# Kernel tuning notes

Measured on AMD Instinct MI355X. Metric: run time of the kernel, lower is better.

The kernel has to match this reference:

```python
import jax, jax.numpy as jnp
import numpy as np

DIM = 768
NUM_HEADS = 16
D_K = DIM // NUM_HEADS


def setup_inputs() -> dict:
    key = jax.random.key(0)
    ks = jax.random.split(key, 9)
    B, T = 4, 2048
    s = 1.0 / np.sqrt(DIM)
    return {
        "x": jax.random.normal(ks[0], (B, T, DIM), dtype=jnp.float32),
        "Wq": jax.random.normal(ks[1], (DIM, DIM), dtype=jnp.float32) * s,
        "bq": jnp.zeros((DIM,), dtype=jnp.float32),
        "Wk": jax.random.normal(ks[2], (DIM, DIM), dtype=jnp.float32) * s,
        "bk": jnp.zeros((DIM,), dtype=jnp.float32),
        "Wv": jax.random.normal(ks[3], (DIM, DIM), dtype=jnp.float32) * s,
        "bv": jnp.zeros((DIM,), dtype=jnp.float32),
        "Wp": jax.random.normal(ks[4], (DIM, DIM), dtype=jnp.float32) * s,
        "bp": jnp.zeros((DIM,), dtype=jnp.float32),
    }


def reference(x, Wq, bq, Wk, bk, Wv, bv, Wp, bp):
    B, T, _ = x.shape
    # QKV projections (weights stored as [in, out])
    q = x @ Wq + bq
    k = x @ Wk + bk
    v = x @ Wv + bv
    # split heads: (B, H, T, d_k)
    q = q.reshape(B, T, NUM_HEADS, D_K).transpose(0, 2, 1, 3)
    k = k.reshape(B, T, NUM_HEADS, D_K).transpose(0, 2, 1, 3)
    v = v.reshape(B, T, NUM_HEADS, D_K).transpose(0, 2, 1, 3)
    # scaled dot-product attention; dropout omitted (eval mode)
    scores = jnp.einsum("bhtd,bhsd->bhts", q, k) / jnp.sqrt(jnp.float32(D_K))
    attn = jax.nn.softmax(scores, axis=-1)
    out = jnp.einsum("bhts,bhsd->bhtd", attn, v)
    out = out.transpose(0, 2, 1, 3).reshape(B, T, DIM)
    return out @ Wp + bp
```

## Files before the change

### kernel.cpp

```cpp
#include <hip/hip_runtime.h>
#include <math.h>

#define T_SEQ 2048
#define B_SZ  4
#define DIM   768
#define NH    16
#define DK    48
#define NQK   1536
#define N3    2304
#define LDP   72

typedef __bf16 bf16x8 __attribute__((ext_vector_type(8)));
typedef float  f32x4  __attribute__((ext_vector_type(4)));

__device__ __forceinline__ unsigned short f32_to_bf16(float f) {
    unsigned u = __float_as_uint(f);
    u += 0x7FFFu + ((u >> 16) & 1u);
    return (unsigned short)(u >> 16);
}
__device__ __forceinline__ unsigned pack_bf16x2(float a, float b) {
    return (unsigned)f32_to_bf16(a) | ((unsigned)f32_to_bf16(b) << 16);
}
__device__ __forceinline__ void lds_dma16(const unsigned short* g, unsigned short* l) {
    __builtin_amdgcn_global_load_lds(
        (const __attribute__((address_space(1))) unsigned int*)g,
        (__attribute__((address_space(3))) unsigned int*)l, 16, 0, 0);
}

__global__ __launch_bounds__(256) void cvt_x_kernel(
    const float* __restrict__ x, unsigned short* __restrict__ xb)
{
    int i = blockIdx.x * 256 + threadIdx.x;
    const float* p = x + (size_t)i * 8;
    float4 f0 = *(const float4*)p;
    float4 f1 = *(const float4*)(p + 4);
    uint4 u;
    u.x = pack_bf16x2(f0.x, f0.y);
    u.y = pack_bf16x2(f0.z, f0.w);
    u.z = pack_bf16x2(f1.x, f1.y);
    u.w = pack_bf16x2(f1.z, f1.w);
    *(uint4*)(xb + (size_t)i * 8) = u;
}

__global__ __launch_bounds__(256) void pack_w_kernel(
    const float* __restrict__ Wq, const float* __restrict__ Wk,
    const float* __restrict__ Wv, const float* __restrict__ Wp,
    unsigned short* __restrict__ Wt, unsigned short* __restrict__ Wpt,
    float qscale)
{
    __shared__ float T[32][33];
    const int mode = blockIdx.z;
    const float* W = (mode == 0) ? Wq : (mode == 1) ? Wk : (mode == 2) ? Wv : Wp;
    const float sc = (mode == 0) ? qscale : 1.0f;
    const int k0 = blockIdx.x * 32, c0 = blockIdx.y * 32;
    const int tx = threadIdx.x & 31, ty = threadIdx.x >> 5;

#pragma unroll
    for (int r = 0; r < 4; ++r) {
        int row = ty + r * 8;
        T[row][tx] = W[(size_t)(k0 + row) * DIM + c0 + tx];
    }
    __syncthreads();
#pragma unroll
    for (int r = 0; r < 4; ++r) {
        int j   = ty + r * 8;
        int col = c0 + j;
        int k   = k0 + tx;
        unsigned short v = f32_to_bf16(T[tx][j] * sc);
        if (mode < 3) Wt[(size_t)(mode * 768 + col) * DIM + k] = v;
        else          Wpt[(size_t)col * DIM + k] = v;
    }
}

__global__ __launch_bounds__(256) void pack_bias_kernel(
    const float* __restrict__ bq, const float* __restrict__ bk,
    const float* __restrict__ bv, float* __restrict__ b3, float qscale)
{
    int n = blockIdx.x * 256 + threadIdx.x;
    if (n >= N3) return;
    float v;
    if (n < 768)       v = bq[n] * qscale;
    else if (n < 1536) v = bk[n - 768];
    else               v = bv[n - 1536];
    b3[n] = v;
}

__global__ __launch_bounds__(256) void gemm_qkv_kernel(
    const unsigned short* __restrict__ A, const unsigned short* __restrict__ Bt,
    const float* __restrict__ bias, unsigned short* __restrict__ QK,
    unsigned short* __restrict__ vT)
{
    __shared__ unsigned short As[128 * 32];
    __shared__ unsigned short Bs[128 * 32];

    const int t = threadIdx.x;
    const int w = t >> 6, lane = t & 63, quad = lane >> 4, lr = lane & 15;
    const int wm = w >> 1, wn = w & 1;
    const int m0 = blockIdx.y * 128, n0 = blockIdx.x * 128;

    const int cw0 = w * 128, cw1 = w * 128 + 64;
    const int ca = cw0 + lane, cb = cw1 + lane;
    const int ra = ca >> 2, sa = (ca & 3) * 8;
    const int rb = cb >> 2, sb = (cb & 3) * 8;

    f32x4 acc[4][4] = {};

    for (int k0 = 0; k0 < DIM; k0 += 32) {
        __syncthreads();
        lds_dma16(A  + (size_t)(m0 + ra) * DIM + k0 + sa, As + cw0 * 8);
        lds_dma16(A  + (size_t)(m0 + rb) * DIM + k0 + sb, As + cw1 * 8);
        lds_dma16(Bt + (size_t)(n0 + ra) * DIM + k0 + sa, Bs + cw0 * 8);
        lds_dma16(Bt + (size_t)(n0 + rb) * DIM + k0 + sb, Bs + cw1 * 8);
        __syncthreads();

        bf16x8 af[4], bfr[4];
#pragma unroll
        for (int mt = 0; mt < 4; ++mt)
            af[mt] = *(const bf16x8*)&As[(wm * 64 + mt * 16 + lr) * 32 + quad * 8];
#pragma unroll
        for (int nt = 0; nt < 4; ++nt)
            bfr[nt] = *(const bf16x8*)&Bs[(wn * 64 + nt * 16 + lr) * 32 + quad * 8];
#pragma unroll
        for (int mt = 0; mt < 4; ++mt)
#pragma unroll
            for (int nt = 0; nt < 4; ++nt)
                acc[mt][nt] = __builtin_amdgcn_mfma_f32_16x16x32_bf16(
                    af[mt], bfr[nt], acc[mt][nt], 0, 0, 0);
    }

    if (blockIdx.x < 12) {
#pragma unroll
        for (int nt = 0; nt < 4; ++nt) {
            int col = n0 + wn * 64 + nt * 16 + lr;
            float bv = bias[col];
#pragma unroll
            for (int mt = 0; mt < 4; ++mt)
#pragma unroll
                for (int r = 0; r < 4; ++r) {
                    int row = m0 + wm * 64 + mt * 16 + quad * 4 + r;
                    QK[(size_t)row * NQK + col] = f32_to_bf16(acc[mt][nt][r] + bv);
                }
        }
    } else {
        const int bidx = m0 >> 11;
        const int ts_base = (m0 & 2047) + wm * 64;
#pragma unroll
        for (int nt = 0; nt < 4; ++nt) {
            int col = n0 + wn * 64 + nt * 16 + lr;
            int vcol = col - 1536;
            int hh = vcol / 48, cc = vcol - hh * 48;
            float bv = bias[col];
            unsigned short* dst0 = vT + ((size_t)(bidx * 16 + hh) * 48 + cc) * T_SEQ;
#pragma unroll
            for (int mt = 0; mt < 4; ++mt) {
                int ts = ts_base + mt * 16 + quad * 4;
                uint2 u;
                u.x = pack_bf16x2(acc[mt][nt][0] + bv, acc[mt][nt][1] + bv);
                u.y = pack_bf16x2(acc[mt][nt][2] + bv, acc[mt][nt][3] + bv);
                *(uint2*)(dst0 + ts) = u;
            }
        }
    }
}

__global__ __launch_bounds__(256) void gemm_out_kernel(
    const unsigned short* __restrict__ A, const unsigned short* __restrict__ Bt,
    const float* __restrict__ bias, float* __restrict__ C)
{
    __shared__ unsigned short As[128 * 32];
    __shared__ unsigned short Bs[128 * 32];

    const int t = threadIdx.x;
    const int w = t >> 6, lane = t & 63, quad = lane >> 4, lr = lane & 15;
    const int wm = w >> 1, wn = w & 1;
    const int m0 = blockIdx.y * 128, n0 = blockIdx.x * 128;

    const int cw0 = w * 128, cw1 = w * 128 + 64;
    const int ca = cw0 + lane, cb = cw1 + lane;
    const int ra = ca >> 2, sa = (ca & 3) * 8;
    const int rb = cb >> 2, sb = (cb & 3) * 8;

    f32x4 acc[4][4] = {};

    for (int k0 = 0; k0 < DIM; k0 += 32) {
        __syncthreads();
        lds_dma16(A  + (size_t)(m0 + ra) * DIM + k0 + sa, As + cw0 * 8);
        lds_dma16(A  + (size_t)(m0 + rb) * DIM + k0 + sb, As + cw1 * 8);
        lds_dma16(Bt + (size_t)(n0 + ra) * DIM + k0 + sa, Bs + cw0 * 8);
        lds_dma16(Bt + (size_t)(n0 + rb) * DIM + k0 + sb, Bs + cw1 * 8);
        __syncthreads();

        bf16x8 af[4], bfr[4];
#pragma unroll
        for (int mt = 0; mt < 4; ++mt)
            af[mt] = *(const bf16x8*)&As[(wm * 64 + mt * 16 + lr) * 32 + quad * 8];
#pragma unroll
        for (int nt = 0; nt < 4; ++nt)
            bfr[nt] = *(const bf16x8*)&Bs[(wn * 64 + nt * 16 + lr) * 32 + quad * 8];
#pragma unroll
        for (int mt = 0; mt < 4; ++mt)
#pragma unroll
            for (int nt = 0; nt < 4; ++nt)
                acc[mt][nt] = __builtin_amdgcn_mfma_f32_16x16x32_bf16(
                    af[mt], bfr[nt], acc[mt][nt], 0, 0, 0);
    }

#pragma unroll
    for (int nt = 0; nt < 4; ++nt) {
        int col = n0 + wn * 64 + nt * 16 + lr;
        float bv = bias[col];
#pragma unroll
        for (int mt = 0; mt < 4; ++mt)
#pragma unroll
            for (int r = 0; r < 4; ++r) {
                int row = m0 + wm * 64 + mt * 16 + quad * 4 + r;
                C[(size_t)row * DIM + col] = acc[mt][nt][r] + bv;
            }
    }
}

__global__ __launch_bounds__(256, 4) void attn_kernel(
    const unsigned short* __restrict__ QK, const unsigned short* __restrict__ vT,
    unsigned short* __restrict__ Ob)
{
    __shared__ unsigned short Ks[64 * 48];
    __shared__ unsigned short Vt[48 * 64];
    __shared__ unsigned short Ps[4 * 32 * LDP];
    __shared__ __align__(16) unsigned short Zs[8];

    const int t = threadIdx.x;
    const int w = t >> 6, lane = t & 63, quad = lane >> 4, lr = lane & 15;
    const int qt = blockIdx.x, h = blockIdx.y, b = blockIdx.z;
    const int base = b * T_SEQ, q0 = qt * 128;
    const int hq = h * DK, hk = 768 + h * DK;
    const int qrow = base + q0 + w * 32;

    if (t < 4) ((unsigned*)Zs)[t] = 0u;

    bf16x8 qa[2], qb[2];
#pragma unroll
    for (int mt = 0; mt < 2; ++mt) {
        const unsigned short* qp = QK + (size_t)(qrow + mt * 16 + lr) * NQK + hq;
        qa[mt] = *(const bf16x8*)(qp + quad * 8);
        qb[mt] = *(const bf16x8*)(qp + 32 + quad * 8);
    }

    const unsigned short* gp[3];
    unsigned short*       lp[3];
    int                   gstep[3];
#pragma unroll
    for (int i = 0; i < 3; ++i) {
        int c = w * 3 + i;
        if (c < 6) {
            int e = c * 512 + lane * 8;
            int r = e / 48, col = e - r * 48;
            gp[i]    = QK + (size_t)(base + r) * NQK + hk + col;
            lp[i]    = Ks + c * 512;
            gstep[i] = 64 * NQK;
        } else {
            int cc = c - 6;
            int e = cc * 512 + lane * 8;
            int d = e >> 6, key = e & 63;
            gp[i]    = vT + ((size_t)(b * NH + h) * DK + d) * T_SEQ + key;
            lp[i]    = Vt + cc * 512;
            gstep[i] = 64;
        }
    }

    f32x4 Oacc[2][3] = {};
    float l_acc[2] = {0.0f, 0.0f};
    unsigned short* Pw = Ps + (w * 32) * LDP;

    for (int kt = 0; kt < T_SEQ / 64; ++kt) {
        __syncthreads();
        lds_dma16(gp[0], lp[0]);
        lds_dma16(gp[1], lp[1]);
        lds_dma16(gp[2], lp[2]);
        gp[0] += gstep[0]; gp[1] += gstep[1]; gp[2] += gstep[2];
        __syncthreads();

        {
            bf16x8 ka[4], kb[4];
#pragma unroll
            for (int nt = 0; nt < 4; ++nt) {
                const unsigned short* kp = Ks + (nt * 16 + lr) * 48;
                ka[nt] = *(const bf16x8*)(kp + quad * 8);
                const unsigned short* kbp = (quad < 2) ? (kp + 32 + quad * 8) : Zs;
                kb[nt] = *(const bf16x8*)kbp;
            }
#pragma unroll
            for (int mt = 0; mt < 2; ++mt) {
                float rs = 0.0f;
#pragma unroll
                for (int nt = 0; nt < 4; ++nt) {
                    f32x4 st = {};
                    st = __builtin_amdgcn_mfma_f32_16x16x32_bf16(ka[nt], qa[mt], st, 0, 0, 0);
                    st = __builtin_amdgcn_mfma_f32_16x16x32_bf16(kb[nt], qb[mt], st, 0, 0, 0);
                    float p0 = __builtin_amdgcn_exp2f(st[0]);
                    float p1 = __builtin_amdgcn_exp2f(st[1]);
                    float p2 = __builtin_amdgcn_exp2f(st[2]);
                    float p3 = __builtin_amdgcn_exp2f(st[3]);
                    rs += (p0 + p1) + (p2 + p3);
                    uint2 pk;
                    pk.x = pack_bf16x2(p0, p1);
                    pk.y = pack_bf16x2(p2, p3);
                    *(uint2*)&Pw[(mt * 16 + lr) * LDP + nt * 16 + quad * 4] = pk;
                }
                rs += __shfl_xor(rs, 16);
                rs += __shfl_xor(rs, 32);
                l_acc[mt] += rs;
            }
        }

        {
            bf16x8 aP[2][2];
#pragma unroll
            for (int mt = 0; mt < 2; ++mt) {
                aP[mt][0] = *(const bf16x8*)&Pw[(mt * 16 + lr) * LDP + quad * 8];
                aP[mt][1] = *(const bf16x8*)&Pw[(mt * 16 + lr) * LDP + 32 + quad * 8];
            }
#pragma unroll
            for (int on = 0; on < 3; ++on) {
                const unsigned short* vp = Vt + (on * 16 + lr) * 64;
                bf16x8 v0 = *(const bf16x8*)(vp + quad * 8);
                bf16x8 v1 = *(const bf16x8*)(vp + 32 + quad * 8);
#pragma unroll
                for (int mt = 0; mt < 2; ++mt) {
                    Oacc[mt][on] = __builtin_amdgcn_mfma_f32_16x16x32_bf16(
                        aP[mt][0], v0, Oacc[mt][on], 0, 0, 0);
                    Oacc[mt][on] = __builtin_amdgcn_mfma_f32_16x16x32_bf16(
                        aP[mt][1], v1, Oacc[mt][on], 0, 0, 0);
                }
            }
        }
    }

#pragma unroll
    for (int mt = 0; mt < 2; ++mt) {
#pragma unroll
        for (int r = 0; r < 4; ++r) {
            float l = __shfl(l_acc[mt], quad * 4 + r);
            float inv = 1.0f / l;
            int row = qrow + mt * 16 + quad * 4 + r;
#pragma unroll
            for (int on = 0; on < 3; ++on)
                Ob[(size_t)row * DIM + h * DK + on * 16 + lr] =
                    f32_to_bf16(Oacc[mt][on][r] * inv);
        }
    }
}

extern "C" void kernel_launch(void* const* d_in, const int* in_sizes, int n_in,
                              void* d_out, int out_size, void* d_ws, size_t ws_size,
                              hipStream_t stream) {
    (void)in_sizes; (void)n_in; (void)out_size; (void)ws_size;

    const float* x  = (const float*)d_in[0];
    const float* Wq = (const float*)d_in[1];
    const float* bq = (const float*)d_in[2];
    const float* Wk = (const float*)d_in[3];
    const float* bk = (const float*)d_in[4];
    const float* Wv = (const float*)d_in[5];
    const float* bv = (const float*)d_in[6];
    const float* Wp = (const float*)d_in[7];
    const float* bp = (const float*)d_in[8];
    float* out = (float*)d_out;

    const size_t M = (size_t)B_SZ * T_SEQ;

    char* ws = (char*)d_ws;
    unsigned short* xb  = (unsigned short*)ws;  ws += M * DIM * 2;
    unsigned short* qk  = (unsigned short*)ws;  ws += M * NQK * 2;
    unsigned short* vT  = (unsigned short*)ws;  ws += M * DIM * 2;
    unsigned short* aob = (unsigned short*)ws;  ws += M * DIM * 2;
    unsigned short* Wt  = (unsigned short*)ws;  ws += (size_t)N3 * DIM * 2;
    unsigned short* Wpt = (unsigned short*)ws;  ws += (size_t)DIM * DIM * 2;
    float*          b3  = (float*)ws;           ws += N3 * 4;

    const float qscale = 0.14433756729740643f * 1.4426950408889634f;

    cvt_x_kernel<<<dim3((int)(M * DIM / 8 / 256)), 256, 0, stream>>>(x, xb);
    pack_w_kernel<<<dim3(DIM / 32, DIM / 32, 4), 256, 0, stream>>>(
        Wq, Wk, Wv, Wp, Wt, Wpt, qscale);
    pack_bias_kernel<<<dim3((N3 + 255) / 256), 256, 0, stream>>>(bq, bk, bv, b3, qscale);

    gemm_qkv_kernel<<<dim3(N3 / 128, (int)(M / 128)), 256, 0, stream>>>(
        xb, Wt, b3, qk, vT);

    attn_kernel<<<dim3(T_SEQ / 128, NH, B_SZ), 256, 0, stream>>>(qk, vT, aob);

    gemm_out_kernel<<<dim3(DIM / 128, (int)(M / 128)), 256, 0, stream>>>(
        aob, Wpt, bp, out);
}
```

Measured before the change: 274.8 us.

## Double-buffer K/V tiles in LDS and pack bf16 probabilities with perm

The attention loop now keeps two LDS buffers for the K and V tiles. It prefetches the next tile through global_load_lds while computing on the current one, which drops one of the two barriers per iteration and overlaps global loads with the MFMA and exp work. Fp32 to bf16 conversion of the softmax probabilities changes from round-to-nearest-even to a cheaper add-0x8000 plus byte-permute sequence. That slightly changes rounding behaviour. The extra buffer doubles the K/V LDS footprint, which could limit occupancy.

```diff
diff --git a/kernel.cpp b/kernel.cpp
--- a/kernel.cpp
+++ b/kernel.cpp
@@ -223,8 +223,7 @@
     const unsigned short* __restrict__ QK, const unsigned short* __restrict__ vT,
     unsigned short* __restrict__ Ob)
 {
-    __shared__ unsigned short Ks[64 * 48];
-    __shared__ unsigned short Vt[48 * 64];
+    __shared__ unsigned short KV[2 * 6144];
     __shared__ unsigned short Ps[4 * 32 * LDP];
     __shared__ __align__(16) unsigned short Zs[8];
 
@@ -234,6 +233,7 @@
     const int base = b * T_SEQ, q0 = qt * 128;
     const int hq = h * DK, hk = 768 + h * DK;
     const int qrow = base + q0 + w * 32;
+    const int NT = T_SEQ / 64;
 
     if (t < 4) ((unsigned*)Zs)[t] = 0u;
 
@@ -246,7 +246,7 @@
     }
 
     const unsigned short* gp[3];
-    unsigned short*       lp[3];
+    unsigned short*       lp0[3];
     int                   gstep[3];
 #pragma unroll
     for (int i = 0; i < 3; ++i) {
@@ -255,35 +255,43 @@
             int e = c * 512 + lane * 8;
             int r = e / 48, col = e - r * 48;
             gp[i]    = QK + (size_t)(base + r) * NQK + hk + col;
-            lp[i]    = Ks + c * 512;
             gstep[i] = 64 * NQK;
         } else {
-            int cc = c - 6;
-            int e = cc * 512 + lane * 8;
+            int e = (c - 6) * 512 + lane * 8;
             int d = e >> 6, key = e & 63;
             gp[i]    = vT + ((size_t)(b * NH + h) * DK + d) * T_SEQ + key;
-            lp[i]    = Vt + cc * 512;
             gstep[i] = 64;
         }
-    }
+        lp0[i] = KV + c * 512;
+    }
+
+    lds_dma16(gp[0], lp0[0]);
+    lds_dma16(gp[1], lp0[1]);
+    lds_dma16(gp[2], lp0[2]);
+    gp[0] += gstep[0]; gp[1] += gstep[1]; gp[2] += gstep[2];
 
     f32x4 Oacc[2][3] = {};
     float l_acc[2] = {0.0f, 0.0f};
     unsigned short* Pw = Ps + (w * 32) * LDP;
 
-    for (int kt = 0; kt < T_SEQ / 64; ++kt) {
+    for (int kt = 0; kt < NT; ++kt) {
+        const int cur = kt & 1;
         __syncthreads();
-        lds_dma16(gp[0], lp[0]);
-        lds_dma16(gp[1], lp[1]);
-        lds_dma16(gp[2], lp[2]);
-        gp[0] += gstep[0]; gp[1] += gstep[1]; gp[2] += gstep[2];
-        __syncthreads();
+        if (kt + 1 < NT) {
+            const int nxt = 6144 - cur * 6144;
+            lds_dma16(gp[0], lp0[0] + nxt);
+            lds_dma16(gp[1], lp0[1] + nxt);
+            lds_dma16(gp[2], lp0[2] + nxt);
+            gp[0] += gstep[0]; gp[1] += gstep[1]; gp[2] += gstep[2];
+        }
+        const unsigned short* Ksb = KV + cur * 6144;
+        const unsigned short* Vtb = Ksb + 3072;
 
         {
             bf16x8 ka[4], kb[4];
 #pragma unroll
             for (int nt = 0; nt < 4; ++nt) {
-                const unsigned short* kp = Ks + (nt * 16 + lr) * 48;
+                const unsigned short* kp = Ksb + (nt * 16 + lr) * 48;
                 ka[nt] = *(const bf16x8*)(kp + quad * 8);
                 const unsigned short* kbp = (quad < 2) ? (kp + 32 + quad * 8) : Zs;
                 kb[nt] = *(const bf16x8*)kbp;
@@ -301,9 +309,13 @@
                     float p2 = __builtin_amdgcn_exp2f(st[2]);
                     float p3 = __builtin_amdgcn_exp2f(st[3]);
                     rs += (p0 + p1) + (p2 + p3);
+                    unsigned u0 = __float_as_uint(p0) + 0x8000u;
+                    unsigned u1 = __float_as_uint(p1) + 0x8000u;
+                    unsigned u2 = __float_as_uint(p2) + 0x8000u;
+                    unsigned u3 = __float_as_uint(p3) + 0x8000u;
                     uint2 pk;
-                    pk.x = pack_bf16x2(p0, p1);
-                    pk.y = pack_bf16x2(p2, p3);
+                    pk.x = __builtin_amdgcn_perm(u1, u0, 0x07060302u);
+                    pk.y = __builtin_amdgcn_perm(u3, u2, 0x07060302u);
                     *(uint2*)&Pw[(mt * 16 + lr) * LDP + nt * 16 + quad * 4] = pk;
                 }
                 rs += __shfl_xor(rs, 16);
@@ -321,7 +333,7 @@
             }
 #pragma unroll
             for (int on = 0; on < 3; ++on) {
-                const unsigned short* vp = Vt + (on * 16 + lr) * 64;
+                const unsigned short* vp = Vtb + (on * 16 + lr) * 64;
                 bf16x8 v0 = *(const bf16x8*)(vp + quad * 8);
                 bf16x8 v1 = *(const bf16x8*)(vp + 32 + quad * 8);
 #pragma unroll
```

Result: no change. 278.4 us (+1.3%).
